# Kernel optimization log

Hardware: AMD Instinct MI355X
Metric: run time of the kernel (lower is better)

Reference implementation:

```python
import jax, jax.numpy as jnp
import numpy as np

IH = IW = 1024          # image size (iH, iW)
NMS_CAND = 1000         # dup_attrs['nms_candidates']
NMS_THR = 0.65          # dup_attrs['nms_thr']
MAX_SEGS = 100          # max_segs


def _mask_to_box(masks):
    # masks: [N, H, W] bool -> xyxy float boxes [N, 4] in pixel coords
    N, H, W = masks.shape
    rows = masks.any(axis=2)            # [N, H]
    cols = masks.any(axis=1)            # [N, W]
    x1 = jnp.argmax(cols, axis=1)
    x2 = W - jnp.argmax(cols[:, ::-1], axis=1)
    y1 = jnp.argmax(rows, axis=1)
    y2 = H - jnp.argmax(rows[:, ::-1], axis=1)
    return jnp.stack([x1, y1, x2, y2], axis=-1).astype(jnp.float32)


def _box_iou(b):
    # b: [K, 4] xyxy -> pairwise IoU [K, K]
    x1, y1, x2, y2 = b[:, 0], b[:, 1], b[:, 2], b[:, 3]
    area = (x2 - x1) * (y2 - y1)
    ix1 = jnp.maximum(x1[:, None], x1[None, :])
    iy1 = jnp.maximum(y1[:, None], y1[None, :])
    ix2 = jnp.minimum(x2[:, None], x2[None, :])
    iy2 = jnp.minimum(y2[:, None], y2[None, :])
    inter = jnp.clip(ix2 - ix1, 0.0) * jnp.clip(iy2 - iy1, 0.0)
    union = area[:, None] + area[None, :] - inter
    return inter / jnp.maximum(union, 1e-9)


def _greedy_nms_keep(iou, thr):
    # boxes assumed pre-sorted by descending score; returns keep mask [K]
    k = iou.shape[0]
    idx = jnp.arange(k)

    def body(i, keep):
        sup = keep[i] & (iou[i] > thr) & (idx > i)
        return keep & ~sup

    return jax.lax.fori_loop(0, k, body, jnp.ones((k,), dtype=bool))


def setup_inputs() -> dict:
    key = jax.random.key(0)
    k1, k2 = jax.random.split(key)
    cls_logits = jax.random.normal(k1, (300, 81), dtype=jnp.float32)
    seg_logits = jax.random.normal(k2, (300, 200, 200), dtype=jnp.float32)
    return {"cls_logits": cls_logits, "seg_logits": seg_logits}


def reference(cls_logits, seg_logits):
    N, fH, fW = seg_logits.shape
    C = cls_logits.shape[1] - 1  # last class is background/no-object

    # mask thresholding + emptiness flag (filtering replaced by score masking)
    pred_masks = seg_logits > 0                              # [N, fH, fW]
    non_empty = pred_masks.reshape(N, -1).sum(axis=1) > 0    # [N]

    # mask -> box for NMS
    boxes = _mask_to_box(pred_masks)                         # [N, 4]

    # sigmoid scoring over (feat, class); empty masks get score -1 (never picked)
    scores = jax.nn.sigmoid(cls_logits[:, :-1])              # [N, C]
    scores = jnp.where(non_empty[:, None], scores, -1.0).reshape(-1)  # [N*C]
    feat_ids = jnp.repeat(jnp.arange(N), C)                  # [N*C]
    labels = jnp.tile(jnp.arange(C), N)                      # [N*C]

    # top nms_candidates (scores sorted descending)
    k = min(NMS_CAND, N * C)
    cand_scores, cand_ids = jax.lax.top_k(scores, k)
    cand_feats = feat_ids[cand_ids]
    cand_labels = labels[cand_ids]
    cand_boxes = boxes[cand_feats]

    # batched (class-aware) NMS: offset boxes per label
    offset = cand_labels.astype(jnp.float32)[:, None] * (float(max(fH, fW)) + 1.0)
    iou = _box_iou(cand_boxes + offset)
    keep = _greedy_nms_keep(iou, NMS_THR) & (cand_scores >= 0.0)

    # keep top max_segs among survivors
    kept_scores = jnp.where(keep, cand_scores, -jnp.inf)
    sel_scores, sel = jax.lax.top_k(kept_scores, MAX_SEGS)
    sel_feats = cand_feats[sel]
    sel_labels = cand_labels[sel]

    # upsample selected mask logits to image size and threshold
    sel_logits = seg_logits[sel_feats]                       # [M, fH, fW]
    maps = jax.image.resize(sel_logits, (MAX_SEGS, IH, IW), method='bilinear')
    out_masks = maps > 0                                     # [M, iH, iW] bool
    batch_ids = jnp.zeros((MAX_SEGS,), dtype=jnp.int32)

    return sel_labels, out_masks, sel_scores, batch_ids
```

## Files before the change

### kernel.cpp

```cpp
#include <hip/hip_runtime.h>
#include <cstdint>
#include <cstddef>

typedef unsigned int u32;
typedef unsigned long long u64;
typedef float vf4 __attribute__((ext_vector_type(4)));

#define NF 300
#define NCLS 80
#define NCLS1 81
#define FH 200
#define FW 200
#define PIX 40000
#define NC 24000
#define KCAND 1000
#define CAP 4096
#define NBINS 65536
#define MAXSEG 100
#define OUT_MASK_OFF 100
#define OUT_SCORE_OFF 104857700
#define OUT_BATCH_OFF 104857800
#define NEG_BIG -3.3895313892515355e38f
#define RYC 16

#define WS_HIST      0u
#define WS_KEYS      262144u
#define WS_COLLECT   454144u
#define WS_CNT       486912u
#define WS_BOXES     486928u
#define WS_CLAB      496928u
#define WS_CFEAT     500928u
#define WS_CSCORE    504928u
#define WS_CBOX      508928u
#define WS_ROWBITS   524928u
#define WS_SELFEAT   656128u

__device__ __forceinline__ u32 ord32_r3(float f) {
  u32 b = __float_as_uint(f);
  return (b & 0x80000000u) ? ~b : (b | 0x80000000u);
}
__device__ __forceinline__ float unord32_r3(u32 o) {
  u32 b = (o & 0x80000000u) ? (o & 0x7FFFFFFFu) : ~o;
  return __uint_as_float(b);
}

__device__ __forceinline__ float4 wcalc_r4(int i) {
  float s = __fsub_rn(__fmul_rn((float)i + 0.5f, 0.1953125f), 0.5f);
  int j0 = (int)floorf(s);
  int j1 = j0 + 1;
  float w0 = fmaxf(0.f, __fsub_rn(1.f, fabsf(__fsub_rn(s, (float)j0))));
  float w1 = fmaxf(0.f, __fsub_rn(1.f, fabsf(__fsub_rn(s, (float)j1))));
  bool in0 = (j0 >= 0) && (j0 < FH);
  bool in1 = (j1 >= 0) && (j1 < FH);
  float tot = __fadd_rn(in0 ? w0 : 0.f, in1 ? w1 : 0.f);
  float w0n = in0 ? (w0 / tot) : 0.f;
  float w1n = in1 ? (w1 / tot) : 0.f;
  return make_float4(w0n, w1n, (float)max(j0, 0), (float)min(j1, FH - 1));
}

__global__ void r5_init(u32* __restrict__ hist, u32* __restrict__ cnts) {
  int i = blockIdx.x * 256 + threadIdx.x;
  hist[i] = 0u;
  if (i < 4) cnts[i] = 0u;
}

__global__ void r5_boxes(const float* __restrict__ seg, const float* __restrict__ cls,
                         float4* __restrict__ boxes, u64* __restrict__ keys,
                         u32* __restrict__ hist) {
  __shared__ int sminx[256], sminy[256], smaxx[256], smaxy[256];
  int n = blockIdx.x, t = threadIdx.x;
  const float4* img = (const float4*)(seg + (size_t)n * PIX);
  int minx = FW, miny = FH, maxx = -1, maxy = -1;
  for (int q = t; q < PIX / 4; q += 256) {
    float4 v = img[q];
    int p = q * 4;
    int y = p / FW;
    int x = p - y * FW;
    if (v.x > 0.f) { minx = min(minx, x);     maxx = max(maxx, x);     miny = min(miny, y); maxy = max(maxy, y); }
    if (v.y > 0.f) { minx = min(minx, x + 1); maxx = max(maxx, x + 1); miny = min(miny, y); maxy = max(maxy, y); }
    if (v.z > 0.f) { minx = min(minx, x + 2); maxx = max(maxx, x + 2); miny = min(miny, y); maxy = max(maxy, y); }
    if (v.w > 0.f) { minx = min(minx, x + 3); maxx = max(maxx, x + 3); miny = min(miny, y); maxy = max(maxy, y); }
  }
  sminx[t] = minx; sminy[t] = miny; smaxx[t] = maxx; smaxy[t] = maxy;
  __syncthreads();
  for (int s = 128; s > 0; s >>= 1) {
    if (t < s) {
      sminx[t] = min(sminx[t], sminx[t + s]);
      sminy[t] = min(sminy[t], sminy[t + s]);
      smaxx[t] = max(smaxx[t], smaxx[t + s]);
      smaxy[t] = max(smaxy[t], smaxy[t + s]);
    }
    __syncthreads();
  }
  bool ne = smaxx[0] >= 0;
  if (t == 0) {
    float4 b;
    if (ne) b = make_float4((float)sminx[0], (float)sminy[0], (float)(smaxx[0] + 1), (float)(smaxy[0] + 1));
    else    b = make_float4(0.f, 0.f, (float)FW, (float)FH);
    boxes[n] = b;
  }
  if (t < NCLS) {
    float sc;
    if (ne) {
      float lg = cls[n * NCLS1 + t];
      sc = 1.0f / (1.0f + expf(-lg));
    } else {
      sc = -1.0f;
    }
    u32 o = ord32_r3(sc);
    u32 i = (u32)(n * NCLS + t);
    keys[i] = ((u64)o << 32) | (u64)(0xFFFFFFFFu - i);
    atomicAdd(&hist[o >> 16], 1u);
  }
}

__global__ void r5_thresh(const u32* __restrict__ hist, u32* __restrict__ cnts) {
  __shared__ u32 s[1024];
  int t = threadIdx.x;
  u32 sum = 0;
  const u32* hp = hist + t * 64;
  for (int b = 0; b < 64; b++) sum += hp[b];
  s[t] = sum;
  __syncthreads();
  for (int off = 1; off < 1024; off <<= 1) {
    u32 v = s[t];
    u32 o = (t + off < 1024) ? s[t + off] : 0u;
    __syncthreads();
    s[t] = v + o;
    __syncthreads();
  }
  u32 sufnext = (t < 1023) ? s[t + 1] : 0u;
  if (s[t] >= (u32)KCAND && sufnext < (u32)KCAND) {
    u32 run = sufnext;
    u32 B = (u32)(t * 64);
    for (int b = 63; b >= 0; b--) {
      run += hist[t * 64 + b];
      if (run >= (u32)KCAND) { B = (u32)(t * 64 + b); break; }
    }
    cnts[1] = B;
  }
}

__global__ void r5_collect(const u64* __restrict__ keys, const u32* __restrict__ cnts,
                           u64* __restrict__ collect, u32* __restrict__ counter) {
  int i = blockIdx.x * 256 + threadIdx.x;
  u32 B = cnts[1];
  bool pass = false;
  u64 k = 0ull;
  if (i < NC) {
    k = keys[i];
    pass = ((u32)(k >> 48) >= B);
  }
  u64 m = __ballot(pass);
  int lane = threadIdx.x & 63;
  u32 base = 0u;
  if (lane == 0 && m) base = atomicAdd(counter, (u32)__popcll(m));
  base = __shfl(base, 0, 64);
  if (pass) {
    u32 pos = base + (u32)__popcll(m & ((1ull << lane) - 1ull));
    if (pos < CAP) collect[pos] = k;
  }
}

__global__ void r5_rank(const u64* __restrict__ collect, const u32* __restrict__ cnts,
                        const float4* __restrict__ boxes,
                        int* __restrict__ clab, int* __restrict__ cfeat,
                        float* __restrict__ cscore, float4* __restrict__ cbox) {
  __shared__ u64 sk[CAP];
  int M = min((int)cnts[0], CAP);
  int t = threadIdx.x;
  for (int j = t; j < M; j += 256) sk[j] = collect[j];
  __syncthreads();
  int j = blockIdx.x * 256 + t;
  if (j < M) {
    u64 my = sk[j];
    int r = 0;
    for (int k = 0; k < M; k++) r += (sk[k] > my) ? 1 : 0;
    if (r < KCAND) {
      u32 idx = 0xFFFFFFFFu - (u32)(my & 0xFFFFFFFFull);
      int n = (int)idx / NCLS, c = (int)idx - n * NCLS;
      clab[r] = c;
      cfeat[r] = n;
      cscore[r] = unord32_r3((u32)(my >> 32));
      float4 b = boxes[n];
      float off = (float)c * 201.0f;
      cbox[r] = make_float4(b.x + off, b.y + off, b.z + off, b.w + off);
    }
  }
}

__global__ void r5_iou(const float4* __restrict__ cbox, u64* __restrict__ rowbits) {
  __shared__ float4 sb[KCAND];
  int t = threadIdx.x;
  for (int j = t; j < KCAND; j += 256) sb[j] = cbox[j];
  __syncthreads();
  int w = t >> 6, lane = t & 63;
  int i = blockIdx.x * 4 + w;
  float4 bi = make_float4(0.f, 0.f, 0.f, 0.f);
  float ai = 0.f;
  if (i < KCAND) { bi = sb[i]; ai = (bi.z - bi.x) * (bi.w - bi.y); }
  for (int ch = 0; ch < 16; ch++) {
    int j = ch * 64 + lane;
    bool pred = false;
    if (i < KCAND && j < KCAND && j > i) {
      float4 bj = sb[j];
      float aj = (bj.z - bj.x) * (bj.w - bj.y);
      float ix1 = fmaxf(bi.x, bj.x), iy1 = fmaxf(bi.y, bj.y);
      float ix2 = fminf(bi.z, bj.z), iy2 = fminf(bi.w, bj.w);
      float inter = fmaxf(ix2 - ix1, 0.f) * fmaxf(iy2 - iy1, 0.f);
      float uni = ai + aj - inter;
      float iou = inter / fmaxf(uni, 1e-9f);
      pred = iou > 0.65f;
    }
    u64 m = __ballot(pred);
    if (lane == 0) rowbits[(size_t)i * 16 + ch] = m;
  }
}

__global__ void r5_nms_sel(const u64* __restrict__ rowbits, const float* __restrict__ cscore,
                           const int* __restrict__ clab, const int* __restrict__ cfeat,
                           float* __restrict__ out, int* __restrict__ selfeat) {
  __shared__ u64 sup[16];
  __shared__ u64 keep[16];
  __shared__ u64 sel[16];
  __shared__ u32 pre[17];
  int t = threadIdx.x;
  if (t < 16) sup[t] = 0ull;
  __syncthreads();
  for (int c = 0; c < 16; c++) {
    if (t < 64) {
      int L = t;
      u64 r = rowbits[(size_t)(c * 64 + L) * 16 + c];
      u64 s = sup[c];
      u64 k = 0ull;
      #pragma unroll 4
      for (int b = 0; b < 64; b++) {
        u64 rb = __shfl(r, b, 64);
        if (!((s >> b) & 1ull)) { s |= rb; k |= (1ull << b); }
      }
      if (L == 0) { sup[c] = s; keep[c] = k; }
      if (L > c && L < 16) {
        u64 acc = sup[L];
        #pragma unroll
        for (int b = 0; b < 64; b++) {
          u64 v = rowbits[(size_t)(c * 64 + b) * 16 + L];
          if ((k >> b) & 1ull) acc |= v;
        }
        sup[L] = acc;
      }
    }
    __syncthreads();
  }
  {
    int w = t >> 6, lane = t & 63;
    bool s = false;
    if (t < KCAND) {
      bool kp = ((keep[t >> 6] >> (t & 63)) & 1ull) != 0ull;
      s = kp && (cscore[t] >= 0.f);
    }
    u64 m = __ballot(s);
    if (lane == 0) sel[w] = m;
  }
  __syncthreads();
  if (t == 0) {
    u32 acc = 0;
    #pragma unroll
    for (int c = 0; c < 16; c++) { pre[c] = acc; acc += (u32)__popcll(sel[c]); }
    pre[16] = acc;
  }
  __syncthreads();
  u32 nkept = pre[16];
  if (t < KCAND) {
    int j = t;
    u64 w = sel[j >> 6];
    bool s = ((w >> (j & 63)) & 1ull) != 0ull;
    u32 below = pre[j >> 6] + (u32)__popcll(w & ((1ull << (j & 63)) - 1ull));
    u32 r = s ? below : (nkept + (u32)j - below);
    if (r < MAXSEG) {
      out[r] = (float)clab[j];
      out[OUT_SCORE_OFF + r] = s ? cscore[j] : NEG_BIG;
      out[OUT_BATCH_OFF + r] = 0.0f;
      selfeat[r] = cfeat[j];
    }
  }
}

__global__ void __launch_bounds__(256) r4_resize(const float* __restrict__ seg,
                                                 const int* __restrict__ selfeat,
                                                 float* __restrict__ outm) {
  __shared__ float srow[6][FW];
  int t = threadIdx.x;
  int yb = blockIdx.x * RYC, slot = blockIdx.y;
  int feat = selfeat[slot];
  const float* img = seg + (size_t)feat * PIX;
  float4 wxa = wcalc_r4(t * 4), wxb = wcalc_r4(t * 4 + 1),
         wxc = wcalc_r4(t * 4 + 2), wxd = wcalc_r4(t * 4 + 3);
  int ylo = (int)wcalc_r4(yb).z;
  int yhi = (int)wcalc_r4(yb + RYC - 1).w;
  int nr = yhi - ylo + 1;
  for (int e = t; e < nr * FW; e += 256) {
    int rr = e / FW, cc = e - rr * FW;
    srow[rr][cc] = img[(ylo + rr) * FW + cc];
  }
  __syncthreads();
  int xb = t * 4;
  int xa0 = (int)wxa.z, xa1 = (int)wxa.w;
  int xb0 = (int)wxb.z, xb1 = (int)wxb.w;
  int xc0 = (int)wxc.z, xc1 = (int)wxc.w;
  int xd0 = (int)wxd.z, xd1 = (int)wxd.w;
  float* obase = outm + (size_t)slot * 1048576 + (size_t)yb * 1024 + xb;
  #pragma unroll
  for (int r = 0; r < RYC; r++) {
    float4 wy = wcalc_r4(yb + r);
    const float* r0 = srow[(int)wy.z - ylo];
    const float* r1 = srow[(int)wy.w - ylo];
    float wy0 = wy.x, wy1 = wy.y;
    float ta0 = __fmaf_rn(wy1, r1[xa0], __fmul_rn(wy0, r0[xa0]));
    float ta1 = __fmaf_rn(wy1, r1[xa1], __fmul_rn(wy0, r0[xa1]));
    float va  = __fmaf_rn(wxa.y, ta1, __fmul_rn(wxa.x, ta0));
    float tb0 = __fmaf_rn(wy1, r1[xb0], __fmul_rn(wy0, r0[xb0]));
    float tb1 = __fmaf_rn(wy1, r1[xb1], __fmul_rn(wy0, r0[xb1]));
    float vb  = __fmaf_rn(wxb.y, tb1, __fmul_rn(wxb.x, tb0));
    float tc0 = __fmaf_rn(wy1, r1[xc0], __fmul_rn(wy0, r0[xc0]));
    float tc1 = __fmaf_rn(wy1, r1[xc1], __fmul_rn(wy0, r0[xc1]));
    float vc  = __fmaf_rn(wxc.y, tc1, __fmul_rn(wxc.x, tc0));
    float td0 = __fmaf_rn(wy1, r1[xd0], __fmul_rn(wy0, r0[xd0]));
    float td1 = __fmaf_rn(wy1, r1[xd1], __fmul_rn(wy0, r0[xd1]));
    float vd  = __fmaf_rn(wxd.y, td1, __fmul_rn(wxd.x, td0));
    vf4 res;
    res.x = (va > 0.0f) ? 1.0f : 0.0f;
    res.y = (vb > 0.0f) ? 1.0f : 0.0f;
    res.z = (vc > 0.0f) ? 1.0f : 0.0f;
    res.w = (vd > 0.0f) ? 1.0f : 0.0f;
    *(vf4*)(obase + (size_t)r * 1024) = res;
  }
}

extern "C" void kernel_launch(void* const* d_in, const int* in_sizes, int n_in,
                              void* d_out, int out_size, void* d_ws, size_t ws_size,
                              hipStream_t stream) {
  const float* cls = (const float*)d_in[0];
  const float* seg = (const float*)d_in[1];
  float* out = (float*)d_out;
  char* ws = (char*)d_ws;

  u32* hist      = (u32*)(ws + WS_HIST);
  u64* keys      = (u64*)(ws + WS_KEYS);
  u64* collect   = (u64*)(ws + WS_COLLECT);
  u32* cnts      = (u32*)(ws + WS_CNT);
  float4* boxes  = (float4*)(ws + WS_BOXES);
  int* clab      = (int*)(ws + WS_CLAB);
  int* cfeat     = (int*)(ws + WS_CFEAT);
  float* cscore  = (float*)(ws + WS_CSCORE);
  float4* cbox   = (float4*)(ws + WS_CBOX);
  u64* rowbits   = (u64*)(ws + WS_ROWBITS);
  int* selfeat   = (int*)(ws + WS_SELFEAT);

  r5_init<<<dim3(NBINS / 256), dim3(256), 0, stream>>>(hist, cnts);
  r5_boxes<<<dim3(NF), dim3(256), 0, stream>>>(seg, cls, boxes, keys, hist);
  r5_thresh<<<dim3(1), dim3(1024), 0, stream>>>(hist, cnts);
  r5_collect<<<dim3((NC + 255) / 256), dim3(256), 0, stream>>>(keys, cnts, collect, &cnts[0]);
  r5_rank<<<dim3(16), dim3(256), 0, stream>>>(collect, cnts, boxes, clab, cfeat, cscore, cbox);
  r5_iou<<<dim3(256), dim3(256), 0, stream>>>(cbox, rowbits);
  r5_nms_sel<<<dim3(1), dim3(1024), 0, stream>>>(rowbits, cscore, clab, cfeat, out, selfeat);
  r4_resize<<<dim3(1024 / RYC, MAXSEG), dim3(256), 0, stream>>>(seg, selfeat, out + OUT_MASK_OFF);
}
```

Before: 602.7 us.

## Fuse IoU bitmask into NMS kernel, computing IoU only for kept boxes

Removes the separate IoU kernel and its global rowbits matrix. NMS now runs in one wavefront that loads candidate boxes and areas into shared memory and, for each surviving box in greedy order, computes IoU against later boxes on the fly via ballots. Only boxes that are kept are processed, which avoids the full 1000x1000 IoU pass and one launch, but the work becomes serialized on a single wave. The histogram threshold kernel also switches to vectorized uint4 loads.

```diff
diff --git a/kernel.cpp b/kernel.cpp
--- a/kernel.cpp
+++ b/kernel.cpp
@@ -32,7 +32,6 @@
 #define WS_CFEAT     500928u
 #define WS_CSCORE    504928u
 #define WS_CBOX      508928u
-#define WS_ROWBITS   524928u
 #define WS_SELFEAT   656128u
 
 __device__ __forceinline__ u32 ord32_r3(float f) {
@@ -114,12 +113,16 @@
   }
 }
 
-__global__ void r5_thresh(const u32* __restrict__ hist, u32* __restrict__ cnts) {
+__global__ void r6_thresh(const u32* __restrict__ hist, u32* __restrict__ cnts) {
   __shared__ u32 s[1024];
   int t = threadIdx.x;
+  const uint4* hp = (const uint4*)(hist) + t * 16;
   u32 sum = 0;
-  const u32* hp = hist + t * 64;
-  for (int b = 0; b < 64; b++) sum += hp[b];
+  #pragma unroll
+  for (int b = 0; b < 16; b++) {
+    uint4 v = hp[b];
+    sum += v.x + v.y + v.z + v.w;
+  }
   s[t] = sum;
   __syncthreads();
   for (int off = 1; off < 1024; off <<= 1) {
@@ -189,73 +192,66 @@
   }
 }
 
-__global__ void r5_iou(const float4* __restrict__ cbox, u64* __restrict__ rowbits) {
-  __shared__ float4 sb[KCAND];
-  int t = threadIdx.x;
-  for (int j = t; j < KCAND; j += 256) sb[j] = cbox[j];
-  __syncthreads();
-  int w = t >> 6, lane = t & 63;
-  int i = blockIdx.x * 4 + w;
-  float4 bi = make_float4(0.f, 0.f, 0.f, 0.f);
-  float ai = 0.f;
-  if (i < KCAND) { bi = sb[i]; ai = (bi.z - bi.x) * (bi.w - bi.y); }
-  for (int ch = 0; ch < 16; ch++) {
-    int j = ch * 64 + lane;
-    bool pred = false;
-    if (i < KCAND && j < KCAND && j > i) {
-      float4 bj = sb[j];
-      float aj = (bj.z - bj.x) * (bj.w - bj.y);
-      float ix1 = fmaxf(bi.x, bj.x), iy1 = fmaxf(bi.y, bj.y);
-      float ix2 = fminf(bi.z, bj.z), iy2 = fminf(bi.w, bj.w);
-      float inter = fmaxf(ix2 - ix1, 0.f) * fmaxf(iy2 - iy1, 0.f);
-      float uni = ai + aj - inter;
-      float iou = inter / fmaxf(uni, 1e-9f);
-      pred = iou > 0.65f;
-    }
-    u64 m = __ballot(pred);
-    if (lane == 0) rowbits[(size_t)i * 16 + ch] = m;
-  }
-}
-
-__global__ void r5_nms_sel(const u64* __restrict__ rowbits, const float* __restrict__ cscore,
+__global__ void r6_nms_sel(const float4* __restrict__ cbox, const float* __restrict__ cscore,
                            const int* __restrict__ clab, const int* __restrict__ cfeat,
                            float* __restrict__ out, int* __restrict__ selfeat) {
-  __shared__ u64 sup[16];
-  __shared__ u64 keep[16];
+  __shared__ float4 sb[1024];
+  __shared__ float sa[1024];
+  __shared__ u64 keepw[16];
   __shared__ u64 sel[16];
   __shared__ u32 pre[17];
   int t = threadIdx.x;
-  if (t < 16) sup[t] = 0ull;
-  __syncthreads();
-  for (int c = 0; c < 16; c++) {
-    if (t < 64) {
-      int L = t;
-      u64 r = rowbits[(size_t)(c * 64 + L) * 16 + c];
-      u64 s = sup[c];
-      u64 k = 0ull;
-      #pragma unroll 4
-      for (int b = 0; b < 64; b++) {
-        u64 rb = __shfl(r, b, 64);
-        if (!((s >> b) & 1ull)) { s |= rb; k |= (1ull << b); }
+  if (t < KCAND) {
+    float4 b = cbox[t];
+    sb[t] = b;
+    sa[t] = (b.z - b.x) * (b.w - b.y);
+  } else {
+    sb[t] = make_float4(0.f, 0.f, 0.f, 0.f);
+    sa[t] = 0.f;
+  }
+  __syncthreads();
+  if (t < 64) {
+    int lane = t;
+    u64 S = 0ull;
+    u64 KW = 0ull;
+    for (int w = 0; w < 16; ++w) {
+      u64 valid = (w == 15) ? ((1ull << (KCAND - 960)) - 1ull) : ~0ull;
+      u64 sw = __shfl(S, w, 64);
+      u64 todo = ~sw & valid;
+      while (todo) {
+        int b = __ffsll((long long)todo) - 1;
+        int i = w * 64 + b;
+        if (lane == w) KW |= (1ull << b);
+        float4 bi = sb[i];
+        float ai = sa[i];
+        for (int ch = w; ch < 16; ++ch) {
+          int j = ch * 64 + lane;
+          bool pred = false;
+          if (j > i && j < KCAND) {
+            float4 bj = sb[j];
+            float ix1 = fmaxf(bi.x, bj.x), iy1 = fmaxf(bi.y, bj.y);
+            float ix2 = fminf(bi.z, bj.z), iy2 = fminf(bi.w, bj.w);
+            float inter = fmaxf(ix2 - ix1, 0.f) * fmaxf(iy2 - iy1, 0.f);
+            float uni = ai + sa[j] - inter;
+            float iou = inter / fmaxf(uni, 1e-9f);
+            pred = iou > 0.65f;
+          }
+          u64 m = __ballot(pred);
+          if (lane == ch) S |= m;
+        }
+        sw = __shfl(S, w, 64);
+        u64 gt = (b == 63) ? 0ull : (~0ull << (b + 1));
+        todo = ~sw & valid & gt;
       }
-      if (L == 0) { sup[c] = s; keep[c] = k; }
-      if (L > c && L < 16) {
-        u64 acc = sup[L];
-        #pragma unroll
-        for (int b = 0; b < 64; b++) {
-          u64 v = rowbits[(size_t)(c * 64 + b) * 16 + L];
-          if ((k >> b) & 1ull) acc |= v;
-        }
-        sup[L] = acc;
-      }
-    }
-    __syncthreads();
-  }
+    }
+    if (lane < 16) keepw[lane] = KW;
+  }
+  __syncthreads();
   {
     int w = t >> 6, lane = t & 63;
     bool s = false;
     if (t < KCAND) {
-      bool kp = ((keep[t >> 6] >> (t & 63)) & 1ull) != 0ull;
+      bool kp = ((keepw[t >> 6] >> (t & 63)) & 1ull) != 0ull;
       s = kp && (cscore[t] >= 0.f);
     }
     u64 m = __ballot(s);
@@ -353,15 +349,13 @@
   int* cfeat     = (int*)(ws + WS_CFEAT);
   float* cscore  = (float*)(ws + WS_CSCORE);
   float4* cbox   = (float4*)(ws + WS_CBOX);
-  u64* rowbits   = (u64*)(ws + WS_ROWBITS);
   int* selfeat   = (int*)(ws + WS_SELFEAT);
 
   r5_init<<<dim3(NBINS / 256), dim3(256), 0, stream>>>(hist, cnts);
   r5_boxes<<<dim3(NF), dim3(256), 0, stream>>>(seg, cls, boxes, keys, hist);
-  r5_thresh<<<dim3(1), dim3(1024), 0, stream>>>(hist, cnts);
+  r6_thresh<<<dim3(1), dim3(1024), 0, stream>>>(hist, cnts);
   r5_collect<<<dim3((NC + 255) / 256), dim3(256), 0, stream>>>(keys, cnts, collect, &cnts[0]);
   r5_rank<<<dim3(16), dim3(256), 0, stream>>>(collect, cnts, boxes, clab, cfeat, cscore, cbox);
-  r5_iou<<<dim3(256), dim3(256), 0, stream>>>(cbox, rowbits);
-  r5_nms_sel<<<dim3(1), dim3(1024), 0, stream>>>(rowbits, cscore, clab, cfeat, out, selfeat);
+  r6_nms_sel<<<dim3(1), dim3(1024), 0, stream>>>(cbox, cscore, clab, cfeat, out, selfeat);
   r4_resize<<<dim3(1024 / RYC, MAXSEG), dim3(256), 0, stream>>>(seg, selfeat, out + OUT_MASK_OFF);
 }
```

New measurement: 723.4 us. +20.0%, slower.

## Parallelize NMS suppression propagation across wavefronts with transposed IoU bitmask

Applied to the files above, without the earlier changes.

The IoU bitmask is stored transposed (chunk-major), so each wavefront of the single-block NMS kernel can load a coalesced row slice for its own later chunk. After wave 0 resolves keep bits for the diagonal chunk, the other wavefronts OR-reduce kept rows with xor shuffles in parallel. Before, one wave looped serially over 64 strided global loads per target chunk. The histogram threshold kernel also switches to vectorized uint4 loads. This adds an extra barrier per chunk, and the rowT buffer must hold 16*1024 entries, which may exceed the old layout's size.

```diff
diff --git a/kernel.cpp b/kernel.cpp
--- a/kernel.cpp
+++ b/kernel.cpp
@@ -114,12 +114,16 @@
   }
 }
 
-__global__ void r5_thresh(const u32* __restrict__ hist, u32* __restrict__ cnts) {
+__global__ void r6_thresh(const u32* __restrict__ hist, u32* __restrict__ cnts) {
   __shared__ u32 s[1024];
   int t = threadIdx.x;
+  const uint4* hp = (const uint4*)(hist) + t * 16;
   u32 sum = 0;
-  const u32* hp = hist + t * 64;
-  for (int b = 0; b < 64; b++) sum += hp[b];
+  #pragma unroll
+  for (int b = 0; b < 16; b++) {
+    uint4 v = hp[b];
+    sum += v.x + v.y + v.z + v.w;
+  }
   s[t] = sum;
   __syncthreads();
   for (int off = 1; off < 1024; off <<= 1) {
@@ -189,7 +193,7 @@
   }
 }
 
-__global__ void r5_iou(const float4* __restrict__ cbox, u64* __restrict__ rowbits) {
+__global__ void r7_iou(const float4* __restrict__ cbox, u64* __restrict__ rowT) {
   __shared__ float4 sb[KCAND];
   int t = threadIdx.x;
   for (int j = t; j < KCAND; j += 256) sb[j] = cbox[j];
@@ -213,11 +217,11 @@
       pred = iou > 0.65f;
     }
     u64 m = __ballot(pred);
-    if (lane == 0) rowbits[(size_t)i * 16 + ch] = m;
-  }
-}
-
-__global__ void r5_nms_sel(const u64* __restrict__ rowbits, const float* __restrict__ cscore,
+    if (lane == 0) rowT[(size_t)ch * 1024 + i] = m;
+  }
+}
+
+__global__ void r7_nms_sel(const u64* __restrict__ rowT, const float* __restrict__ cscore,
                            const int* __restrict__ clab, const int* __restrict__ cfeat,
                            float* __restrict__ out, int* __restrict__ selfeat) {
   __shared__ u64 sup[16];
@@ -225,41 +229,41 @@
   __shared__ u64 sel[16];
   __shared__ u32 pre[17];
   int t = threadIdx.x;
+  int wv = t >> 6, lane = t & 63;
   if (t < 16) sup[t] = 0ull;
   __syncthreads();
   for (int c = 0; c < 16; c++) {
-    if (t < 64) {
-      int L = t;
-      u64 r = rowbits[(size_t)(c * 64 + L) * 16 + c];
+    u64 row = 0ull;
+    if (wv > c) row = rowT[(size_t)wv * 1024 + c * 64 + lane];
+    if (wv == 0) {
+      u64 r = rowT[(size_t)c * 1024 + c * 64 + lane];
       u64 s = sup[c];
       u64 k = 0ull;
-      #pragma unroll 4
+      #pragma unroll
       for (int b = 0; b < 64; b++) {
         u64 rb = __shfl(r, b, 64);
         if (!((s >> b) & 1ull)) { s |= rb; k |= (1ull << b); }
       }
-      if (L == 0) { sup[c] = s; keep[c] = k; }
-      if (L > c && L < 16) {
-        u64 acc = sup[L];
-        #pragma unroll
-        for (int b = 0; b < 64; b++) {
-          u64 v = rowbits[(size_t)(c * 64 + b) * 16 + L];
-          if ((k >> b) & 1ull) acc |= v;
-        }
-        sup[L] = acc;
-      }
+      if (lane == 0) keep[c] = k;
+    }
+    __syncthreads();
+    if (wv > c) {
+      u64 kk = keep[c];
+      u64 acc = ((kk >> lane) & 1ull) ? row : 0ull;
+      #pragma unroll
+      for (int off = 32; off >= 1; off >>= 1) acc |= __shfl_xor(acc, off, 64);
+      if (lane == 0) sup[wv] |= acc;
     }
     __syncthreads();
   }
   {
-    int w = t >> 6, lane = t & 63;
     bool s = false;
     if (t < KCAND) {
       bool kp = ((keep[t >> 6] >> (t & 63)) & 1ull) != 0ull;
       s = kp && (cscore[t] >= 0.f);
     }
     u64 m = __ballot(s);
-    if (lane == 0) sel[w] = m;
+    if (lane == 0) sel[wv] = m;
   }
   __syncthreads();
   if (t == 0) {
@@ -353,15 +357,15 @@
   int* cfeat     = (int*)(ws + WS_CFEAT);
   float* cscore  = (float*)(ws + WS_CSCORE);
   float4* cbox   = (float4*)(ws + WS_CBOX);
-  u64* rowbits   = (u64*)(ws + WS_ROWBITS);
+  u64* rowT      = (u64*)(ws + WS_ROWBITS);
   int* selfeat   = (int*)(ws + WS_SELFEAT);
 
   r5_init<<<dim3(NBINS / 256), dim3(256), 0, stream>>>(hist, cnts);
   r5_boxes<<<dim3(NF), dim3(256), 0, stream>>>(seg, cls, boxes, keys, hist);
-  r5_thresh<<<dim3(1), dim3(1024), 0, stream>>>(hist, cnts);
+  r6_thresh<<<dim3(1), dim3(1024), 0, stream>>>(hist, cnts);
   r5_collect<<<dim3((NC + 255) / 256), dim3(256), 0, stream>>>(keys, cnts, collect, &cnts[0]);
   r5_rank<<<dim3(16), dim3(256), 0, stream>>>(collect, cnts, boxes, clab, cfeat, cscore, cbox);
-  r5_iou<<<dim3(256), dim3(256), 0, stream>>>(cbox, rowbits);
-  r5_nms_sel<<<dim3(1), dim3(1024), 0, stream>>>(rowbits, cscore, clab, cfeat, out, selfeat);
+  r7_iou<<<dim3(256), dim3(256), 0, stream>>>(cbox, rowT);
+  r7_nms_sel<<<dim3(1), dim3(1024), 0, stream>>>(rowT, cscore, clab, cfeat, out, selfeat);
   r4_resize<<<dim3(1024 / RYC, MAXSEG), dim3(256), 0, stream>>>(seg, selfeat, out + OUT_MASK_OFF);
 }
```

Result: faster. 559.0 us (-7.2%).
